# Optimization experiments

Hardware: AMD Instinct MI355X
Metric: run time of the kernel (lower is better)

The kernel has to match this reference:

```python
import jax, jax.numpy as jnp
import numpy as np

N = 100000   # nodes
E = 3200000  # edges
D = 128      # in_channels
H = 128      # subhiddens
O = 128      # out_channels
S = 2048     # subgraphs
EPS = 1e-5


def _glorot(k, shape):
    lim = np.sqrt(6.0 / (shape[0] + shape[1])).astype(np.float32)
    return jax.random.uniform(k, shape, jnp.float32, -lim, lim)


def setup_inputs() -> dict:
    key = jax.random.key(0)
    ks = jax.random.split(key, 8)
    x = jax.random.normal(ks[0], (N, D), jnp.float32)
    edge_index = jax.random.randint(ks[1], (2, E), 0, N, dtype=jnp.int32)
    node_to_subgraph = jnp.sort(jax.random.randint(ks[2], (N,), 0, S, dtype=jnp.int32))
    return {
        "x": x,
        "edge_index": edge_index,
        "node_to_subgraph": node_to_subgraph,
        "W1": _glorot(ks[3], (D, H)), "b1": jnp.zeros((H,), jnp.float32),
        "g1": jnp.ones((H,), jnp.float32), "be1": jnp.zeros((H,), jnp.float32),
        "W2": _glorot(ks[4], (H, H)), "b2": jnp.zeros((H,), jnp.float32),
        "g2": jnp.ones((H,), jnp.float32), "be2": jnp.zeros((H,), jnp.float32),
        "W3": _glorot(ks[5], (H, O)), "b3": jnp.zeros((O,), jnp.float32),
    }


def _gcn_conv(x, W, b, row, col, norm):
    # PyG GCNConv: out[col] += norm * (x @ W)[row], then + bias.
    xw = x @ W                                    # [N+?, d] -> [N, d_out]
    msg = xw[row] * norm[:, None]                 # gather over source nodes
    out = jax.ops.segment_sum(msg, col, num_segments=N)
    return out + b


def _bn_relu(x, g, be):
    # BatchNorm1d (training-mode batch stats, biased var) + ReLU
    mean = jnp.mean(x, axis=0)
    var = jnp.mean(jnp.square(x - mean), axis=0)
    return jax.nn.relu((x - mean) * jax.lax.rsqrt(var + EPS) * g + be)


def reference(x, edge_index, node_to_subgraph, W1, b1, g1, be1, W2, b2, g2, be2, W3, b3):
    # GCN symmetric norm with self-loops, shared across the 3 convs.
    loops = jnp.arange(N, dtype=edge_index.dtype)
    row = jnp.concatenate([edge_index[0], loops])  # source
    col = jnp.concatenate([edge_index[1], loops])  # target (aggregation)
    deg = jax.ops.segment_sum(jnp.ones_like(col, dtype=x.dtype), col, num_segments=N)
    dinv = jnp.where(deg > 0, jax.lax.rsqrt(deg), 0.0)
    norm = dinv[row] * dinv[col]

    h1 = _bn_relu(_gcn_conv(x, W1, b1, row, col, norm), g1, be1)   # dropout is no-op in eval
    h2 = _bn_relu(_gcn_conv(h1, W2, b2, row, col, norm), g2, be2)
    h3 = jax.nn.relu(_gcn_conv(h2, W3, b3, row, col, norm))

    cat = jnp.concatenate([h1, h2, h3], axis=-1)                   # [N, 2H+O]
    return jax.ops.segment_max(cat, node_to_subgraph, num_segments=S)  # gmp -> [S, 2H+O]
```

## Files before the change

kernel.cpp:

```cpp
#include <hip/hip_runtime.h>
#include <hip/hip_fp16.h>

#define NN 100000
#define NE 3200000
#define DF 128
#define SG 2048
#define OUTC 384
#define EPS 1e-5f

#define NBUK 800
#define BNODES 125
#define CAP 5120
#define TILE 4096
#define B_BUCKET 782
#define B_GEMM 391
#define LDSTRIDE 136
#define AGG_BLOCKS 2048
#define AGG_WAVES (AGG_BLOCKS * 4)
#define CHUNK 13

typedef _Float16 f16x8 __attribute__((ext_vector_type(8)));
typedef float f32x16 __attribute__((ext_vector_type(16)));

__global__ void k_init(const float* __restrict__ W1, const float* __restrict__ W2,
                       const float* __restrict__ W3, __half* __restrict__ WT,
                       unsigned int* __restrict__ outz, int* __restrict__ gcur,
                       float* __restrict__ sums) {
    int g = blockIdx.x * 256 + threadIdx.x;
    int nt = gridDim.x * 256;
    for (int i = g; i < SG * OUTC; i += nt) outz[i] = 0u;
    if (g < NBUK) gcur[g] = 0;
    if (g < 512) sums[g] = 0.f;
    for (int i = g; i < 3 * 16384; i += nt) {
        int m = i >> 14, idx = i & 16383;
        int k = idx >> 7, n = idx & 127;
        const float* W = m == 0 ? W1 : (m == 1 ? W2 : W3);
        WT[m * 16384 + n * 128 + k] = __float2half(W[idx]);
    }
}

__device__ void bucketA_body(int* smem, int bb,
                             const int* __restrict__ erow, const int* __restrict__ ecol,
                             int* __restrict__ gcur, int* __restrict__ packed) {
    int* sc   = smem;
    int* sr   = smem + 4096;
    int* hist = smem + 8192;
    int* loff = smem + 9216;
    int* gch  = smem + 10240;
    int* cur  = smem + 11264;
    int* psum = smem + 12288;
    int t = threadIdx.x;
    hist[t] = 0; hist[t + 256] = 0; hist[t + 512] = 0; hist[t + 768] = 0;
    __syncthreads();
    int e0 = bb * TILE;
    int lim = NE - e0; if (lim > TILE) lim = TILE;
    for (int i = t; i < lim; i += 256) {
        int c = ecol[e0 + i];
        int r = erow[e0 + i];
        sc[i] = c; sr[i] = r;
        atomicAdd(&hist[c / BNODES], 1);
    }
    __syncthreads();
    int h0 = hist[4 * t], h1 = hist[4 * t + 1], h2 = hist[4 * t + 2], h3 = hist[4 * t + 3];
    int s = h0 + h1 + h2 + h3;
    psum[t] = s; __syncthreads();
    for (int st = 1; st < 256; st <<= 1) {
        int a = (t >= st) ? psum[t - st] : 0;
        __syncthreads();
        psum[t] += a;
        __syncthreads();
    }
    int base = psum[t] - s;
    loff[4 * t] = base;
    loff[4 * t + 1] = base + h0;
    loff[4 * t + 2] = base + h0 + h1;
    loff[4 * t + 3] = base + h0 + h1 + h2;
#pragma unroll
    for (int j = 0; j < 4; ++j) {
        int b = 4 * t + j;
        if (b < NBUK) {
            int c = hist[b];
            gch[b] = c ? atomicAdd(&gcur[b], c) : 0;
            cur[b] = loff[b];
        }
    }
    __syncthreads();
    for (int i = t; i < lim; i += 256) {
        int c = sc[i], r = sr[i];
        int b = c / BNODES;
        int lc = c - b * BNODES;
        int p = atomicAdd(&cur[b], 1);
        int rank = p - loff[b];
        if (gch[b] + rank < CAP) packed[b * CAP + gch[b] + rank] = r | (lc << 17);
    }
}

__device__ void gemm32u_body(int* smem, int gb, const float* __restrict__ A,
                             const __half* __restrict__ WTg, __half* __restrict__ C) {
    _Float16* Wl = (_Float16*)smem;
    int tid = threadIdx.x;
    for (int ch = tid; ch < 2048; ch += 256) {
        int n = ch >> 4, seg = ch & 15;
        *(uint4*)&Wl[n * LDSTRIDE + seg * 8] = *(const uint4*)(WTg + n * 128 + seg * 8);
    }
    __syncthreads();
    int wave = tid >> 6, lane = tid & 63;
    int l31 = lane & 31, lhi = lane >> 5;
    int rowbase = gb * 256 + wave * 64;
    f32x16 acc[2][4];
#pragma unroll
    for (int rt = 0; rt < 2; ++rt)
#pragma unroll
        for (int nt = 0; nt < 4; ++nt)
#pragma unroll
            for (int i = 0; i < 16; ++i) acc[rt][nt][i] = 0.f;
    int r0 = rowbase + l31;      if (r0 >= NN) r0 = NN - 1;
    int r1 = rowbase + 32 + l31; if (r1 >= NN) r1 = NN - 1;
    const float* A0 = A + (size_t)r0 * 128;
    const float* A1 = A + (size_t)r1 * 128;
#pragma unroll
    for (int ks = 0; ks < 8; ++ks) {
        int koff = ks * 16 + lhi * 8;
        float4 f0 = *(const float4*)(A0 + koff);
        float4 f1 = *(const float4*)(A0 + koff + 4);
        float4 g0 = *(const float4*)(A1 + koff);
        float4 g1 = *(const float4*)(A1 + koff + 4);
        f16x8 a0, a1;
        a0[0] = (_Float16)f0.x; a0[1] = (_Float16)f0.y; a0[2] = (_Float16)f0.z; a0[3] = (_Float16)f0.w;
        a0[4] = (_Float16)f1.x; a0[5] = (_Float16)f1.y; a0[6] = (_Float16)f1.z; a0[7] = (_Float16)f1.w;
        a1[0] = (_Float16)g0.x; a1[1] = (_Float16)g0.y; a1[2] = (_Float16)g0.z; a1[3] = (_Float16)g0.w;
        a1[4] = (_Float16)g1.x; a1[5] = (_Float16)g1.y; a1[6] = (_Float16)g1.z; a1[7] = (_Float16)g1.w;
#pragma unroll
        for (int nt = 0; nt < 4; ++nt) {
            f16x8 b = *(const f16x8*)&Wl[(nt * 32 + l31) * LDSTRIDE + ks * 16 + lhi * 8];
            acc[0][nt] = __builtin_amdgcn_mfma_f32_32x32x16_f16(a0, b, acc[0][nt], 0, 0, 0);
            acc[1][nt] = __builtin_amdgcn_mfma_f32_32x32x16_f16(a1, b, acc[1][nt], 0, 0, 0);
        }
    }
#pragma unroll
    for (int rt = 0; rt < 2; ++rt) {
#pragma unroll
        for (int r = 0; r < 16; ++r) {
            int row = rowbase + rt * 32 + (r & 3) + 8 * (r >> 2) + 4 * lhi;
            if (row < NN) {
                size_t cb = (size_t)row * 128 + l31;
                C[cb]      = __float2half(acc[rt][0][r]);
                C[cb + 32] = __float2half(acc[rt][1][r]);
                C[cb + 64] = __float2half(acc[rt][2][r]);
                C[cb + 96] = __float2half(acc[rt][3][r]);
            }
        }
    }
}

__global__ __launch_bounds__(256, 2) void k_fused1(const int* __restrict__ erow,
                                                   const int* __restrict__ ecol,
                                                   int* __restrict__ gcur,
                                                   int* __restrict__ packed,
                                                   const float* __restrict__ x,
                                                   const __half* __restrict__ WT,
                                                   __half* __restrict__ XWh) {
    __shared__ __align__(16) int smem[12544];
    int bb = blockIdx.x;
    if (bb < B_BUCKET) bucketA_body(smem, bb, erow, ecol, gcur, packed);
    else gemm32u_body(smem, bb - B_BUCKET, x, WT, XWh);
}

__global__ __launch_bounds__(256) void k_csrB(int* __restrict__ rows,
                                              const int* __restrict__ gcur,
                                              int* __restrict__ begs, int* __restrict__ ends,
                                              float* __restrict__ dinv,
                                              __half* __restrict__ XWh) {
    __shared__ int lin[CAP];
    __shared__ int hist[128], off[128], cur[128], psc[128];
    __shared__ float dinvl[128];
    int b = blockIdx.x, t = threadIdx.x;
    int cnt = gcur[b]; if (cnt > CAP) cnt = CAP;
    int base = b * CAP;
    for (int i = t; i < cnt; i += 256) lin[i] = rows[base + i];
    if (t < 128) hist[t] = 0;
    __syncthreads();
    for (int i = t; i < cnt; i += 256) atomicAdd(&hist[lin[i] >> 17], 1);
    __syncthreads();
    int pc = 0;
    if (t < 128) { pc = (hist[t] + 3) & ~3; psc[t] = pc; }
    __syncthreads();
    for (int st = 1; st < 128; st <<= 1) {
        int a = 0;
        if (t < 128 && t >= st) a = psc[t - st];
        __syncthreads();
        if (t < 128) psc[t] += a;
        __syncthreads();
    }
    if (t < 128) { off[t] = psc[t] - pc; cur[t] = off[t]; }
    __syncthreads();
    if (t < BNODES) {
        int n = b * BNODES + t;
        int c = hist[t];
        int bg = base + off[t];
        begs[n] = bg;
        ends[n] = bg + c;
        float dv = rsqrtf((float)(c + 1));
        dinv[n] = dv;
        dinvl[t] = dv;
        int pad = (c + 3) & ~3;
        for (int p = c; p < pad; ++p)
            if (off[t] + p < CAP) rows[base + off[t] + p] = 0;
    }
    __syncthreads();
    for (int i = t; i < cnt; i += 256) {
        int w = lin[i];
        int lc = w >> 17;
        int p = atomicAdd(&cur[lc], 1);
        if (p < CAP) rows[base + p] = w & 0x1FFFF;
    }
    int rr = t >> 1, half = t & 1;
    if (rr < BNODES) {
        float dv = dinvl[rr];
        int n = b * BNODES + rr;
        uint4* p = (uint4*)(XWh + (size_t)n * 128) + half * 8;
#pragma unroll
        for (int j = 0; j < 8; ++j) {
            uint4 v = p[j];
            __half2* h = (__half2*)&v;
#pragma unroll
            for (int q = 0; q < 4; ++q) {
                float2 f = __half22float2(h[q]);
                h[q] = __floats2half2_rn(f.x * dv, f.y * dv);
            }
            p[j] = v;
        }
    }
}

__global__ __launch_bounds__(256, 2) void k_gemm16(const __half* __restrict__ A,
                                                   const __half* __restrict__ WTg,
                                                   const float* __restrict__ dinv,
                                                   __half* __restrict__ C) {
    __shared__ _Float16 Wl[128 * LDSTRIDE];
    int tid = threadIdx.x;
    for (int ch = tid; ch < 2048; ch += 256) {
        int n = ch >> 4, seg = ch & 15;
        *(uint4*)&Wl[n * LDSTRIDE + seg * 8] = *(const uint4*)(WTg + n * 128 + seg * 8);
    }
    __syncthreads();
    int wave = tid >> 6, lane = tid & 63;
    int l31 = lane & 31, lhi = lane >> 5;
    int rowbase = blockIdx.x * 256 + wave * 64;
    f32x16 acc[2][4];
#pragma unroll
    for (int rt = 0; rt < 2; ++rt)
#pragma unroll
        for (int nt = 0; nt < 4; ++nt)
#pragma unroll
            for (int i = 0; i < 16; ++i) acc[rt][nt][i] = 0.f;
    int r0 = rowbase + l31;      if (r0 >= NN) r0 = NN - 1;
    int r1 = rowbase + 32 + l31; if (r1 >= NN) r1 = NN - 1;
    const f16x8* A0 = (const f16x8*)(A + (size_t)r0 * 128);
    const f16x8* A1 = (const f16x8*)(A + (size_t)r1 * 128);
#pragma unroll
    for (int ks = 0; ks < 8; ++ks) {
        f16x8 a0 = A0[ks * 2 + lhi];
        f16x8 a1 = A1[ks * 2 + lhi];
#pragma unroll
        for (int nt = 0; nt < 4; ++nt) {
            f16x8 b = *(const f16x8*)&Wl[(nt * 32 + l31) * LDSTRIDE + ks * 16 + lhi * 8];
            acc[0][nt] = __builtin_amdgcn_mfma_f32_32x32x16_f16(a0, b, acc[0][nt], 0, 0, 0);
            acc[1][nt] = __builtin_amdgcn_mfma_f32_32x32x16_f16(a1, b, acc[1][nt], 0, 0, 0);
        }
    }
#pragma unroll
    for (int rt = 0; rt < 2; ++rt) {
#pragma unroll
        for (int r = 0; r < 16; ++r) {
            int row = rowbase + rt * 32 + (r & 3) + 8 * (r >> 2) + 4 * lhi;
            if (row < NN) {
                float sc = dinv[row];
                size_t cb = (size_t)row * 128 + l31;
                C[cb]      = __float2half(acc[rt][0][r] * sc);
                C[cb + 32] = __float2half(acc[rt][1][r] * sc);
                C[cb + 64] = __float2half(acc[rt][2][r] * sc);
                C[cb + 96] = __float2half(acc[rt][3][r] * sc);
            }
        }
    }
}

__device__ __forceinline__ void accum8(float* acc, uint4 v) {
    float2 f;
    f = __half22float2(*(__half2*)&v.x); acc[0] += f.x; acc[1] += f.y;
    f = __half22float2(*(__half2*)&v.y); acc[2] += f.x; acc[3] += f.y;
    f = __half22float2(*(__half2*)&v.z); acc[4] += f.x; acc[5] += f.y;
    f = __half22float2(*(__half2*)&v.w); acc[6] += f.x; acc[7] += f.y;
}
__device__ __forceinline__ void accum8w(float* acc, uint4 v, float w) {
    float2 f;
    f = __half22float2(*(__half2*)&v.x); acc[0] = fmaf(w, f.x, acc[0]); acc[1] = fmaf(w, f.y, acc[1]);
    f = __half22float2(*(__half2*)&v.y); acc[2] = fmaf(w, f.x, acc[2]); acc[3] = fmaf(w, f.y, acc[3]);
    f = __half22float2(*(__half2*)&v.z); acc[4] = fmaf(w, f.x, acc[4]); acc[5] = fmaf(w, f.y, acc[5]);
    f = __half22float2(*(__half2*)&v.w); acc[6] = fmaf(w, f.x, acc[6]); acc[7] = fmaf(w, f.y, acc[7]);
}

__device__ __forceinline__ void agg_node(const uint4* __restrict__ XW4,
                                         const int* __restrict__ rows,
                                         int n, int beg, int end, int quad, int li,
                                         float* acc) {
#pragma unroll
    for (int j = 0; j < 8; ++j) acc[j] = 0.f;
    if (quad == 0) {
        uint4 sv = XW4[(size_t)n * 16 + li];
        accum8(acc, sv);
    }
    int e = beg;
    for (; e + 32 <= end; e += 32) {
        int4 ia = *(const int4*)(rows + e + 4 * quad);
        int4 ib = *(const int4*)(rows + e + 16 + 4 * quad);
        uint4 v0 = XW4[(size_t)ia.x * 16 + li];
        uint4 v1 = XW4[(size_t)ia.y * 16 + li];
        uint4 v2 = XW4[(size_t)ia.z * 16 + li];
        uint4 v3 = XW4[(size_t)ia.w * 16 + li];
        uint4 v4 = XW4[(size_t)ib.x * 16 + li];
        uint4 v5 = XW4[(size_t)ib.y * 16 + li];
        uint4 v6 = XW4[(size_t)ib.z * 16 + li];
        uint4 v7 = XW4[(size_t)ib.w * 16 + li];
        accum8(acc, v0); accum8(acc, v1); accum8(acc, v2); accum8(acc, v3);
        accum8(acc, v4); accum8(acc, v5); accum8(acc, v6); accum8(acc, v7);
    }
    for (; e + 16 <= end; e += 16) {
        int4 ia = *(const int4*)(rows + e + 4 * quad);
        uint4 v0 = XW4[(size_t)ia.x * 16 + li];
        uint4 v1 = XW4[(size_t)ia.y * 16 + li];
        uint4 v2 = XW4[(size_t)ia.z * 16 + li];
        uint4 v3 = XW4[(size_t)ia.w * 16 + li];
        accum8(acc, v0); accum8(acc, v1); accum8(acc, v2); accum8(acc, v3);
    }
    if (e < end) {
        int rem = end - e;
        int qb = 4 * quad;
        int4 it = make_int4(0, 0, 0, 0);
        if (qb < rem) it = *(const int4*)(rows + e + qb);
        uint4 v0 = XW4[(size_t)it.x * 16 + li];
        uint4 v1 = XW4[(size_t)it.y * 16 + li];
        uint4 v2 = XW4[(size_t)it.z * 16 + li];
        uint4 v3 = XW4[(size_t)it.w * 16 + li];
        accum8w(acc, v0, (qb + 0 < rem) ? 1.f : 0.f);
        accum8w(acc, v1, (qb + 1 < rem) ? 1.f : 0.f);
        accum8w(acc, v2, (qb + 2 < rem) ? 1.f : 0.f);
        accum8w(acc, v3, (qb + 3 < rem) ? 1.f : 0.f);
    }
#pragma unroll
    for (int j = 0; j < 8; ++j) {
        acc[j] += __shfl_xor(acc[j], 16, 64);
        acc[j] += __shfl_xor(acc[j], 32, 64);
    }
}

__global__ __launch_bounds__(256) void k_agghs(const __half* __restrict__ XWh,
                                               const int* __restrict__ begs,
                                               const int* __restrict__ ends,
                                               const int* __restrict__ rows,
                                               const float* __restrict__ dinv,
                                               __half* __restrict__ outh,
                                               float* __restrict__ sums) {
    __shared__ float sred[4][256];
    int wave = threadIdx.x >> 6, lane = threadIdx.x & 63;
    int quad = lane >> 4, li = lane & 15;
    const uint4* XW4 = (const uint4*)XWh;
    int wid = blockIdx.x * 4 + wave;
    int n0 = wid * CHUNK;
    int n1 = n0 + CHUNK; if (n1 > NN) n1 = NN;
    float ssum[8] = {}, sqsum[8] = {};
    for (int n = n0; n < n1; ++n) {
        float acc[8];
        agg_node(XW4, rows, n, begs[n], ends[n], quad, li, acc);
        if (quad == 0) {
            float dn = dinv[n];
            __half2 hh[4];
#pragma unroll
            for (int j = 0; j < 8; ++j) {
                float v = acc[j] * dn;
                acc[j] = v;
                ssum[j] += v;
                sqsum[j] += v * v;
            }
            hh[0] = __floats2half2_rn(acc[0], acc[1]);
            hh[1] = __floats2half2_rn(acc[2], acc[3]);
            hh[2] = __floats2half2_rn(acc[4], acc[5]);
            hh[3] = __floats2half2_rn(acc[6], acc[7]);
            *(uint4*)(outh + (size_t)n * 128 + li * 8) = *(uint4*)hh;
        }
    }
    if (quad == 0) {
#pragma unroll
        for (int j = 0; j < 8; ++j) {
            sred[wave][li * 8 + j] = ssum[j];
            sred[wave][128 + li * 8 + j] = sqsum[j];
        }
    }
    __syncthreads();
    int t = threadIdx.x;
    float tot = sred[0][t] + sred[1][t] + sred[2][t] + sred[3][t];
    atomicAdd(&sums[t], tot);
}

__global__ __launch_bounds__(256) void k_agghmax(const __half* __restrict__ XWh,
                                                 const int* __restrict__ begs,
                                                 const int* __restrict__ ends,
                                                 const int* __restrict__ rows,
                                                 const float* __restrict__ dinv,
                                                 const float* __restrict__ b3,
                                                 const int* __restrict__ n2s,
                                                 unsigned int* __restrict__ outmax) {
    int wave = threadIdx.x >> 6, lane = threadIdx.x & 63;
    int quad = lane >> 4, li = lane & 15;
    const uint4* XW4 = (const uint4*)XWh;
    int wid = blockIdx.x * 4 + wave;
    int n0 = wid * CHUNK;
    int n1 = n0 + CHUNK; if (n1 > NN) n1 = NN;
    float4 bz0 = *(const float4*)(b3 + li * 8);
    float4 bz1 = *(const float4*)(b3 + li * 8 + 4);
    float bias[8] = {bz0.x, bz0.y, bz0.z, bz0.w, bz1.x, bz1.y, bz1.z, bz1.w};
    int cur = -1;
    float runmax[8];
    for (int n = n0; n < n1; ++n) {
        float acc[8];
        agg_node(XW4, rows, n, begs[n], ends[n], quad, li, acc);
        float dn = dinv[n];
        int sg = n2s[n];
        if (sg != cur) {
            if (cur >= 0 && quad == 0) {
#pragma unroll
                for (int j = 0; j < 8; ++j)
                    atomicMax(&outmax[cur * OUTC + 256 + li * 8 + j], __float_as_uint(runmax[j]));
            }
            cur = sg;
#pragma unroll
            for (int j = 0; j < 8; ++j) runmax[j] = fmaxf(acc[j] * dn + bias[j], 0.f);
        } else {
#pragma unroll
            for (int j = 0; j < 8; ++j) runmax[j] = fmaxf(runmax[j], fmaxf(acc[j] * dn + bias[j], 0.f));
        }
    }
    if (cur >= 0 && quad == 0) {
#pragma unroll
        for (int j = 0; j < 8; ++j)
            atomicMax(&outmax[cur * OUTC + 256 + li * 8 + j], __float_as_uint(runmax[j]));
    }
}

__global__ void k_bnmax(__half* __restrict__ buf, const float* __restrict__ sums,
                        const float* __restrict__ g, const float* __restrict__ be,
                        const int* __restrict__ n2s,
                        unsigned int* __restrict__ outmax, int colOff) {
    int c = threadIdx.x & 127;
    int rg = threadIdx.x >> 7;
    int n0 = blockIdx.x * 64;
    int nEnd = n0 + 64; if (nEnd > NN) nEnd = NN;
    float mean = sums[c] * (1.0f / NN);
    float inv = rsqrtf(sums[128 + c] * (1.0f / NN) - mean * mean + EPS) * g[c];
    float sc = inv, sh = be[c] - mean * inv;
    int cur = -1; float runmax = 0.f;
    for (int n = n0 + rg; n < nEnd; n += 2) {
        float v = fmaxf(__half2float(buf[(size_t)n * 128 + c]) * sc + sh, 0.f);
        buf[(size_t)n * 128 + c] = __float2half(v);
        int sg = n2s[n];
        if (sg != cur) {
            if (cur >= 0) atomicMax(&outmax[cur * OUTC + colOff + c], __float_as_uint(runmax));
            cur = sg; runmax = v;
        } else {
            runmax = fmaxf(runmax, v);
        }
    }
    if (cur >= 0) atomicMax(&outmax[cur * OUTC + colOff + c], __float_as_uint(runmax));
}

extern "C" void kernel_launch(void* const* d_in, const int* in_sizes, int n_in,
                              void* d_out, int out_size, void* d_ws, size_t ws_size,
                              hipStream_t stream) {
    const float* x   = (const float*)d_in[0];
    const int*   ei  = (const int*)d_in[1];
    const int*   n2s = (const int*)d_in[2];
    const float* W1  = (const float*)d_in[3];
    const float* g1  = (const float*)d_in[5];
    const float* be1 = (const float*)d_in[6];
    const float* W2  = (const float*)d_in[7];
    const float* g2  = (const float*)d_in[9];
    const float* be2 = (const float*)d_in[10];
    const float* W3  = (const float*)d_in[11];
    const float* b3  = (const float*)d_in[12];

    __half* H    = (__half*)d_ws;
    __half* XWh  = H + (size_t)NN * 128;
    __half* WT   = XWh + (size_t)NN * 128;
    int* rows    = (int*)(WT + 3 * 16384);
    int* begs    = rows + (size_t)NBUK * CAP;
    int* ends    = begs + NN;
    float* dinv  = (float*)(ends + NN);
    int* gcur    = (int*)(dinv + NN);
    float* sums  = (float*)(gcur + NBUK);

    const int* erow = ei;
    const int* ecol = ei + NE;
    unsigned int* outmax = (unsigned int*)d_out;
    int nbSeg = (NN + 63) / 64;
    int nbG = (NN + 255) / 256;

    k_init<<<512, 256, 0, stream>>>(W1, W2, W3, WT, outmax, gcur, sums);
    k_fused1<<<B_BUCKET + B_GEMM, 256, 0, stream>>>(erow, ecol, gcur, rows, x, WT, XWh);
    k_csrB<<<NBUK, 256, 0, stream>>>(rows, gcur, begs, ends, dinv, XWh);

    k_agghs<<<AGG_BLOCKS, 256, 0, stream>>>(XWh, begs, ends, rows, dinv, H, sums);
    k_bnmax<<<nbSeg, 256, 0, stream>>>(H, sums, g1, be1, n2s, outmax, 0);

    k_gemm16<<<nbG, 256, 0, stream>>>(H, WT + 16384, dinv, XWh);
    k_agghs<<<AGG_BLOCKS, 256, 0, stream>>>(XWh, begs, ends, rows, dinv, H, sums + 256);
    k_bnmax<<<nbSeg, 256, 0, stream>>>(H, sums + 256, g2, be2, n2s, outmax, 128);

    k_gemm16<<<nbG, 256, 0, stream>>>(H, WT + 32768, dinv, XWh);
    k_agghmax<<<AGG_BLOCKS, 256, 0, stream>>>(XWh, begs, ends, rows, dinv, b3, n2s, outmax);
}
```

Before: 705.4 us.

## Store XW in column panels and aggregate per-panel with XCC-affine chunk claiming

The GEMM outputs are now written in a panel-major layout: 8 panels of 16 columns, each panel contiguous over all nodes. The aggregation kernels are rewritten so each block claims a chunk of nodes for one panel through atomic counters, preferring the panel matching its XCC id. The aim is for each XCC's L2 to hold only a 3.2MB panel slice during the random gather instead of the full 25.6MB feature matrix. The cost is 8x more passes over the edge index lists and narrower per-lane gathers (4 bytes).

```diff
diff --git a/kernel.cpp b/kernel.cpp
--- a/kernel.cpp
+++ b/kernel.cpp
@@ -3,7 +3,6 @@
 
 #define NN 100000
 #define NE 3200000
-#define DF 128
 #define SG 2048
 #define OUTC 384
 #define EPS 1e-5f
@@ -15,9 +14,12 @@
 #define B_BUCKET 782
 #define B_GEMM 391
 #define LDSTRIDE 136
-#define AGG_BLOCKS 2048
-#define AGG_WAVES (AGG_BLOCKS * 4)
-#define CHUNK 13
+
+#define NPAN 8
+#define CPP 256
+#define CHUNKP 98
+#define CHKB (4 * CHUNKP)
+#define AGGP_GRID 4096
 
 typedef _Float16 f16x8 __attribute__((ext_vector_type(8)));
 typedef float f32x16 __attribute__((ext_vector_type(16)));
@@ -25,12 +27,13 @@
 __global__ void k_init(const float* __restrict__ W1, const float* __restrict__ W2,
                        const float* __restrict__ W3, __half* __restrict__ WT,
                        unsigned int* __restrict__ outz, int* __restrict__ gcur,
-                       float* __restrict__ sums) {
+                       float* __restrict__ sums, int* __restrict__ ctrs) {
     int g = blockIdx.x * 256 + threadIdx.x;
     int nt = gridDim.x * 256;
     for (int i = g; i < SG * OUTC; i += nt) outz[i] = 0u;
     if (g < NBUK) gcur[g] = 0;
     if (g < 512) sums[g] = 0.f;
+    if (g < 24) ctrs[g] = 0;
     for (int i = g; i < 3 * 16384; i += nt) {
         int m = i >> 14, idx = i & 16383;
         int k = idx >> 7, n = idx & 127;
@@ -95,6 +98,10 @@
     }
 }
 
+__device__ __forceinline__ void panel_store(__half* __restrict__ C, int row, int col, float v) {
+    C[((size_t)(col >> 4) * NN + row) * 16 + (col & 15)] = __float2half(v);
+}
+
 __device__ void gemm32u_body(int* smem, int gb, const float* __restrict__ A,
                              const __half* __restrict__ WTg, __half* __restrict__ C) {
     _Float16* Wl = (_Float16*)smem;
@@ -143,11 +150,9 @@
         for (int r = 0; r < 16; ++r) {
             int row = rowbase + rt * 32 + (r & 3) + 8 * (r >> 2) + 4 * lhi;
             if (row < NN) {
-                size_t cb = (size_t)row * 128 + l31;
-                C[cb]      = __float2half(acc[rt][0][r]);
-                C[cb + 32] = __float2half(acc[rt][1][r]);
-                C[cb + 64] = __float2half(acc[rt][2][r]);
-                C[cb + 96] = __float2half(acc[rt][3][r]);
+#pragma unroll
+                for (int nt = 0; nt < 4; ++nt)
+                    panel_store(C, row, nt * 32 + l31, acc[rt][nt][r]);
             }
         }
     }
@@ -159,18 +164,18 @@
                                                    int* __restrict__ packed,
                                                    const float* __restrict__ x,
                                                    const __half* __restrict__ WT,
-                                                   __half* __restrict__ XWh) {
+                                                   __half* __restrict__ XWp) {
     __shared__ __align__(16) int smem[12544];
     int bb = blockIdx.x;
     if (bb < B_BUCKET) bucketA_body(smem, bb, erow, ecol, gcur, packed);
-    else gemm32u_body(smem, bb - B_BUCKET, x, WT, XWh);
+    else gemm32u_body(smem, bb - B_BUCKET, x, WT, XWp);
 }
 
 __global__ __launch_bounds__(256) void k_csrB(int* __restrict__ rows,
                                               const int* __restrict__ gcur,
                                               int* __restrict__ begs, int* __restrict__ ends,
                                               float* __restrict__ dinv,
-                                              __half* __restrict__ XWh) {
+                                              __half* __restrict__ XWp) {
     __shared__ int lin[CAP];
     __shared__ int hist[128], off[128], cur[128], psc[128];
     __shared__ float dinvl[128];
@@ -214,21 +219,21 @@
         int p = atomicAdd(&cur[lc], 1);
         if (p < CAP) rows[base + p] = w & 0x1FFFF;
     }
-    int rr = t >> 1, half = t & 1;
+    int rr = t >> 1, hf = t & 1;
     if (rr < BNODES) {
         float dv = dinvl[rr];
-        int n = b * BNODES + rr;
-        uint4* p = (uint4*)(XWh + (size_t)n * 128) + half * 8;
-#pragma unroll
-        for (int j = 0; j < 8; ++j) {
-            uint4 v = p[j];
+        size_t n = (size_t)b * BNODES + rr;
+#pragma unroll
+        for (int p = 0; p < NPAN; ++p) {
+            uint4* q = (uint4*)(XWp + ((size_t)p * NN + n) * 16) + hf;
+            uint4 v = *q;
             __half2* h = (__half2*)&v;
 #pragma unroll
-            for (int q = 0; q < 4; ++q) {
-                float2 f = __half22float2(h[q]);
-                h[q] = __floats2half2_rn(f.x * dv, f.y * dv);
+            for (int qq = 0; qq < 4; ++qq) {
+                float2 f = __half22float2(h[qq]);
+                h[qq] = __floats2half2_rn(f.x * dv, f.y * dv);
             }
-            p[j] = v;
+            *q = v;
         }
     }
 }
@@ -276,175 +281,157 @@
             int row = rowbase + rt * 32 + (r & 3) + 8 * (r >> 2) + 4 * lhi;
             if (row < NN) {
                 float sc = dinv[row];
-                size_t cb = (size_t)row * 128 + l31;
-                C[cb]      = __float2half(acc[rt][0][r] * sc);
-                C[cb + 32] = __float2half(acc[rt][1][r] * sc);
-                C[cb + 64] = __float2half(acc[rt][2][r] * sc);
-                C[cb + 96] = __float2half(acc[rt][3][r] * sc);
+#pragma unroll
+                for (int nt = 0; nt < 4; ++nt)
+                    panel_store(C, row, nt * 32 + l31, acc[rt][nt][r] * sc);
             }
         }
     }
 }
 
-__device__ __forceinline__ void accum8(float* acc, uint4 v) {
-    float2 f;
-    f = __half22float2(*(__half2*)&v.x); acc[0] += f.x; acc[1] += f.y;
-    f = __half22float2(*(__half2*)&v.y); acc[2] += f.x; acc[3] += f.y;
-    f = __half22float2(*(__half2*)&v.z); acc[4] += f.x; acc[5] += f.y;
-    f = __half22float2(*(__half2*)&v.w); acc[6] += f.x; acc[7] += f.y;
-}
-__device__ __forceinline__ void accum8w(float* acc, uint4 v, float w) {
-    float2 f;
-    f = __half22float2(*(__half2*)&v.x); acc[0] = fmaf(w, f.x, acc[0]); acc[1] = fmaf(w, f.y, acc[1]);
-    f = __half22float2(*(__half2*)&v.y); acc[2] = fmaf(w, f.x, acc[2]); acc[3] = fmaf(w, f.y, acc[3]);
-    f = __half22float2(*(__half2*)&v.z); acc[4] = fmaf(w, f.x, acc[4]); acc[5] = fmaf(w, f.y, acc[5]);
-    f = __half22float2(*(__half2*)&v.w); acc[6] = fmaf(w, f.x, acc[6]); acc[7] = fmaf(w, f.y, acc[7]);
-}
-
-__device__ __forceinline__ void agg_node(const uint4* __restrict__ XW4,
-                                         const int* __restrict__ rows,
-                                         int n, int beg, int end, int quad, int li,
-                                         float* acc) {
-#pragma unroll
-    for (int j = 0; j < 8; ++j) acc[j] = 0.f;
-    if (quad == 0) {
-        uint4 sv = XW4[(size_t)n * 16 + li];
-        accum8(acc, sv);
-    }
-    int e = beg;
-    for (; e + 32 <= end; e += 32) {
-        int4 ia = *(const int4*)(rows + e + 4 * quad);
-        int4 ib = *(const int4*)(rows + e + 16 + 4 * quad);
-        uint4 v0 = XW4[(size_t)ia.x * 16 + li];
-        uint4 v1 = XW4[(size_t)ia.y * 16 + li];
-        uint4 v2 = XW4[(size_t)ia.z * 16 + li];
-        uint4 v3 = XW4[(size_t)ia.w * 16 + li];
-        uint4 v4 = XW4[(size_t)ib.x * 16 + li];
-        uint4 v5 = XW4[(size_t)ib.y * 16 + li];
-        uint4 v6 = XW4[(size_t)ib.z * 16 + li];
-        uint4 v7 = XW4[(size_t)ib.w * 16 + li];
-        accum8(acc, v0); accum8(acc, v1); accum8(acc, v2); accum8(acc, v3);
-        accum8(acc, v4); accum8(acc, v5); accum8(acc, v6); accum8(acc, v7);
-    }
-    for (; e + 16 <= end; e += 16) {
-        int4 ia = *(const int4*)(rows + e + 4 * quad);
-        uint4 v0 = XW4[(size_t)ia.x * 16 + li];
-        uint4 v1 = XW4[(size_t)ia.y * 16 + li];
-        uint4 v2 = XW4[(size_t)ia.z * 16 + li];
-        uint4 v3 = XW4[(size_t)ia.w * 16 + li];
-        accum8(acc, v0); accum8(acc, v1); accum8(acc, v2); accum8(acc, v3);
-    }
-    if (e < end) {
-        int rem = end - e;
-        int qb = 4 * quad;
-        int4 it = make_int4(0, 0, 0, 0);
-        if (qb < rem) it = *(const int4*)(rows + e + qb);
-        uint4 v0 = XW4[(size_t)it.x * 16 + li];
-        uint4 v1 = XW4[(size_t)it.y * 16 + li];
-        uint4 v2 = XW4[(size_t)it.z * 16 + li];
-        uint4 v3 = XW4[(size_t)it.w * 16 + li];
-        accum8w(acc, v0, (qb + 0 < rem) ? 1.f : 0.f);
-        accum8w(acc, v1, (qb + 1 < rem) ? 1.f : 0.f);
-        accum8w(acc, v2, (qb + 2 < rem) ? 1.f : 0.f);
-        accum8w(acc, v3, (qb + 3 < rem) ? 1.f : 0.f);
-    }
-#pragma unroll
-    for (int j = 0; j < 8; ++j) {
-        acc[j] += __shfl_xor(acc[j], 16, 64);
-        acc[j] += __shfl_xor(acc[j], 32, 64);
-    }
-}
-
-__global__ __launch_bounds__(256) void k_agghs(const __half* __restrict__ XWh,
-                                               const int* __restrict__ begs,
-                                               const int* __restrict__ ends,
-                                               const int* __restrict__ rows,
-                                               const float* __restrict__ dinv,
-                                               __half* __restrict__ outh,
-                                               float* __restrict__ sums) {
-    __shared__ float sred[4][256];
-    int wave = threadIdx.x >> 6, lane = threadIdx.x & 63;
-    int quad = lane >> 4, li = lane & 15;
-    const uint4* XW4 = (const uint4*)XWh;
-    int wid = blockIdx.x * 4 + wave;
-    int n0 = wid * CHUNK;
-    int n1 = n0 + CHUNK; if (n1 > NN) n1 = NN;
-    float ssum[8] = {}, sqsum[8] = {};
-    for (int n = n0; n < n1; ++n) {
-        float acc[8];
-        agg_node(XW4, rows, n, begs[n], ends[n], quad, li, acc);
-        if (quad == 0) {
-            float dn = dinv[n];
-            __half2 hh[4];
-#pragma unroll
-            for (int j = 0; j < 8; ++j) {
-                float v = acc[j] * dn;
-                acc[j] = v;
-                ssum[j] += v;
-                sqsum[j] += v * v;
+__device__ __forceinline__ void claim_chunk(int* ctr, int* s_chunk, int* s_panel) {
+    if (threadIdx.x == 0) {
+        int xcc = __builtin_amdgcn_s_getreg((3 << 11) | 20) & 7;
+        int pnl = xcc;
+        int c = atomicAdd(&ctr[pnl], 1);
+        if (c >= CPP) {
+            for (int d = 1; d < 8; ++d) {
+                pnl = (xcc + d) & 7;
+                c = atomicAdd(&ctr[pnl], 1);
+                if (c < CPP) break;
             }
-            hh[0] = __floats2half2_rn(acc[0], acc[1]);
-            hh[1] = __floats2half2_rn(acc[2], acc[3]);
-            hh[2] = __floats2half2_rn(acc[4], acc[5]);
-            hh[3] = __floats2half2_rn(acc[6], acc[7]);
-            *(uint4*)(outh + (size_t)n * 128 + li * 8) = *(uint4*)hh;
-        }
-    }
-    if (quad == 0) {
-#pragma unroll
-        for (int j = 0; j < 8; ++j) {
-            sred[wave][li * 8 + j] = ssum[j];
-            sred[wave][128 + li * 8 + j] = sqsum[j];
-        }
-    }
-    __syncthreads();
-    int t = threadIdx.x;
-    float tot = sred[0][t] + sred[1][t] + sred[2][t] + sred[3][t];
-    atomicAdd(&sums[t], tot);
-}
-
-__global__ __launch_bounds__(256) void k_agghmax(const __half* __restrict__ XWh,
+        }
+        *s_chunk = (c < CPP) ? c : -1;
+        *s_panel = pnl;
+    }
+}
+
+__device__ __forceinline__ float2 aggp_node(const unsigned int* __restrict__ XW2,
+                                            const int* __restrict__ rows,
+                                            size_t pbase, int n, int beg, int end,
+                                            int lg, int cc) {
+    float2 acc = make_float2(0.f, 0.f);
+    if (lg == 0) {
+        unsigned int sv = XW2[(pbase + n) * 8 + cc];
+        float2 f = __half22float2(*(__half2*)&sv);
+        acc.x += f.x; acc.y += f.y;
+    }
+    for (int e = beg; e < end; e += 64) {
+        unsigned int vg[8];
+#pragma unroll
+        for (int g = 0; g < 8; ++g) {
+            vg[g] = 0u;
+            if (e + g * 8 < end) {
+                int idx = e + g * 8 + lg;
+                bool val = idx < end;
+                int r = val ? rows[idx] : 0;
+                unsigned int v = XW2[(pbase + r) * 8 + cc];
+                vg[g] = val ? v : 0u;
+            }
+        }
+#pragma unroll
+        for (int g = 0; g < 8; ++g) {
+            float2 f = __half22float2(*(__half2*)&vg[g]);
+            acc.x += f.x; acc.y += f.y;
+        }
+    }
+    acc.x += __shfl_xor(acc.x, 8, 64);  acc.y += __shfl_xor(acc.y, 8, 64);
+    acc.x += __shfl_xor(acc.x, 16, 64); acc.y += __shfl_xor(acc.y, 16, 64);
+    acc.x += __shfl_xor(acc.x, 32, 64); acc.y += __shfl_xor(acc.y, 32, 64);
+    return acc;
+}
+
+__global__ __launch_bounds__(256, 8) void k_aggp(const __half* __restrict__ XWp,
                                                  const int* __restrict__ begs,
                                                  const int* __restrict__ ends,
                                                  const int* __restrict__ rows,
                                                  const float* __restrict__ dinv,
-                                                 const float* __restrict__ b3,
-                                                 const int* __restrict__ n2s,
-                                                 unsigned int* __restrict__ outmax) {
+                                                 __half* __restrict__ H,
+                                                 float* __restrict__ sums,
+                                                 int* __restrict__ ctr) {
+    __shared__ int s_chunk, s_panel;
+    __shared__ float sred[4][32];
+    claim_chunk(ctr, &s_chunk, &s_panel);
+    __syncthreads();
+    int chunk = s_chunk;
+    if (chunk < 0) return;
+    int p = s_panel;
     int wave = threadIdx.x >> 6, lane = threadIdx.x & 63;
-    int quad = lane >> 4, li = lane & 15;
-    const uint4* XW4 = (const uint4*)XWh;
-    int wid = blockIdx.x * 4 + wave;
-    int n0 = wid * CHUNK;
-    int n1 = n0 + CHUNK; if (n1 > NN) n1 = NN;
-    float4 bz0 = *(const float4*)(b3 + li * 8);
-    float4 bz1 = *(const float4*)(b3 + li * 8 + 4);
-    float bias[8] = {bz0.x, bz0.y, bz0.z, bz0.w, bz1.x, bz1.y, bz1.z, bz1.w};
+    int lg = lane >> 3, cc = lane & 7;
+    const unsigned int* XW2 = (const unsigned int*)XWp;
+    size_t pbase = (size_t)p * NN;
+    int n0 = chunk * CHKB + wave * CHUNKP;
+    int n1 = n0 + CHUNKP; if (n1 > NN) n1 = NN;
+    float2 ssum = make_float2(0.f, 0.f), sqsum = make_float2(0.f, 0.f);
+    for (int n = n0; n < n1; ++n) {
+        float2 acc = aggp_node(XW2, rows, pbase, n, begs[n], ends[n], lg, cc);
+        if (lg == 0) {
+            float dn = dinv[n];
+            float vx = acc.x * dn, vy = acc.y * dn;
+            __half2 hh = __floats2half2_rn(vx, vy);
+            ((unsigned int*)H)[(size_t)n * 64 + p * 8 + cc] = *(unsigned int*)&hh;
+            ssum.x += vx; ssum.y += vy;
+            sqsum.x += vx * vx; sqsum.y += vy * vy;
+        }
+    }
+    if (lg == 0) {
+        sred[wave][cc * 2] = ssum.x;  sred[wave][cc * 2 + 1] = ssum.y;
+        sred[wave][16 + cc * 2] = sqsum.x; sred[wave][16 + cc * 2 + 1] = sqsum.y;
+    }
+    __syncthreads();
+    int t = threadIdx.x;
+    if (t < 32) {
+        float v = sred[0][t] + sred[1][t] + sred[2][t] + sred[3][t];
+        int col = p * 16 + (t & 15);
+        atomicAdd(&sums[(t < 16 ? 0 : 128) + col], v);
+    }
+}
+
+__global__ __launch_bounds__(256, 8) void k_aggpmax(const __half* __restrict__ XWp,
+                                                    const int* __restrict__ begs,
+                                                    const int* __restrict__ ends,
+                                                    const int* __restrict__ rows,
+                                                    const float* __restrict__ dinv,
+                                                    const float* __restrict__ b3,
+                                                    const int* __restrict__ n2s,
+                                                    unsigned int* __restrict__ outmax,
+                                                    int* __restrict__ ctr) {
+    __shared__ int s_chunk, s_panel;
+    claim_chunk(ctr, &s_chunk, &s_panel);
+    __syncthreads();
+    int chunk = s_chunk;
+    if (chunk < 0) return;
+    int p = s_panel;
+    int wave = threadIdx.x >> 6, lane = threadIdx.x & 63;
+    int lg = lane >> 3, cc = lane & 7;
+    const unsigned int* XW2 = (const unsigned int*)XWp;
+    size_t pbase = (size_t)p * NN;
+    int n0 = chunk * CHKB + wave * CHUNKP;
+    int n1 = n0 + CHUNKP; if (n1 > NN) n1 = NN;
+    float2 bias = make_float2(b3[p * 16 + cc * 2], b3[p * 16 + cc * 2 + 1]);
     int cur = -1;
-    float runmax[8];
+    float2 runm = make_float2(0.f, 0.f);
     for (int n = n0; n < n1; ++n) {
-        float acc[8];
-        agg_node(XW4, rows, n, begs[n], ends[n], quad, li, acc);
+        float2 acc = aggp_node(XW2, rows, pbase, n, begs[n], ends[n], lg, cc);
         float dn = dinv[n];
+        float vx = fmaxf(acc.x * dn + bias.x, 0.f);
+        float vy = fmaxf(acc.y * dn + bias.y, 0.f);
         int sg = n2s[n];
         if (sg != cur) {
-            if (cur >= 0 && quad == 0) {
-#pragma unroll
-                for (int j = 0; j < 8; ++j)
-                    atomicMax(&outmax[cur * OUTC + 256 + li * 8 + j], __float_as_uint(runmax[j]));
+            if (cur >= 0 && lg == 0) {
+                atomicMax(&outmax[cur * OUTC + 256 + p * 16 + cc * 2], __float_as_uint(runm.x));
+                atomicMax(&outmax[cur * OUTC + 256 + p * 16 + cc * 2 + 1], __float_as_uint(runm.y));
             }
             cur = sg;
-#pragma unroll
-            for (int j = 0; j < 8; ++j) runmax[j] = fmaxf(acc[j] * dn + bias[j], 0.f);
+            runm.x = vx; runm.y = vy;
         } else {
-#pragma unroll
-            for (int j = 0; j < 8; ++j) runmax[j] = fmaxf(runmax[j], fmaxf(acc[j] * dn + bias[j], 0.f));
-        }
-    }
-    if (cur >= 0 && quad == 0) {
-#pragma unroll
-        for (int j = 0; j < 8; ++j)
-            atomicMax(&outmax[cur * OUTC + 256 + li * 8 + j], __float_as_uint(runmax[j]));
+            runm.x = fmaxf(runm.x, vx);
+            runm.y = fmaxf(runm.y, vy);
+        }
+    }
+    if (cur >= 0 && lg == 0) {
+        atomicMax(&outmax[cur * OUTC + 256 + p * 16 + cc * 2], __float_as_uint(runm.x));
+        atomicMax(&outmax[cur * OUTC + 256 + p * 16 + cc * 2 + 1], __float_as_uint(runm.y));
     }
 }
 
@@ -490,14 +477,15 @@
     const float* b3  = (const float*)d_in[12];
 
     __half* H    = (__half*)d_ws;
-    __half* XWh  = H + (size_t)NN * 128;
-    __half* WT   = XWh + (size_t)NN * 128;
+    __half* XWp  = H + (size_t)NN * 128;
+    __half* WT   = XWp + (size_t)NN * 128;
     int* rows    = (int*)(WT + 3 * 16384);
     int* begs    = rows + (size_t)NBUK * CAP;
     int* ends    = begs + NN;
     float* dinv  = (float*)(ends + NN);
     int* gcur    = (int*)(dinv + NN);
     float* sums  = (float*)(gcur + NBUK);
+    int* ctrs    = (int*)(sums + 512);
 
     const int* erow = ei;
     const int* ecol = ei + NE;
@@ -505,17 +493,17 @@
     int nbSeg = (NN + 63) / 64;
     int nbG = (NN + 255) / 256;
 
-    k_init<<<512, 256, 0, stream>>>(W1, W2, W3, WT, outmax, gcur, sums);
-    k_fused1<<<B_BUCKET + B_GEMM, 256, 0, stream>>>(erow, ecol, gcur, rows, x, WT, XWh);
-    k_csrB<<<NBUK, 256, 0, stream>>>(rows, gcur, begs, ends, dinv, XWh);
-
-    k_agghs<<<AGG_BLOCKS, 256, 0, stream>>>(XWh, begs, ends, rows, dinv, H, sums);
+    k_init<<<512, 256, 0, stream>>>(W1, W2, W3, WT, outmax, gcur, sums, ctrs);
+    k_fused1<<<B_BUCKET + B_GEMM, 256, 0, stream>>>(erow, ecol, gcur, rows, x, WT, XWp);
+    k_csrB<<<NBUK, 256, 0, stream>>>(rows, gcur, begs, ends, dinv, XWp);
+
+    k_aggp<<<AGGP_GRID, 256, 0, stream>>>(XWp, begs, ends, rows, dinv, H, sums, ctrs);
     k_bnmax<<<nbSeg, 256, 0, stream>>>(H, sums, g1, be1, n2s, outmax, 0);
 
-    k_gemm16<<<nbG, 256, 0, stream>>>(H, WT + 16384, dinv, XWh);
-    k_agghs<<<AGG_BLOCKS, 256, 0, stream>>>(XWh, begs, ends, rows, dinv, H, sums + 256);
+    k_gemm16<<<nbG, 256, 0, stream>>>(H, WT + 16384, dinv, XWp);
+    k_aggp<<<AGGP_GRID, 256, 0, stream>>>(XWp, begs, ends, rows, dinv, H, sums + 256, ctrs + 8);
     k_bnmax<<<nbSeg, 256, 0, stream>>>(H, sums + 256, g2, be2, n2s, outmax, 128);
 
-    k_gemm16<<<nbG, 256, 0, stream>>>(H, WT + 32768, dinv, XWh);
-    k_agghmax<<<AGG_BLOCKS, 256, 0, stream>>>(XWh, begs, ends, rows, dinv, b3, n2s, outmax);
-}
+    k_gemm16<<<nbG, 256, 0, stream>>>(H, WT + 32768, dinv, XWp);
+    k_aggpmax<<<AGGP_GRID, 256, 0, stream>>>(XWp, begs, ends, rows, dinv, b3, n2s, outmax, ctrs + 16);
+}
```

After: 1.883 ms. +166.9%, slower.
